# Optimization experiments

Hardware: AMD Instinct MI355X
Metric: run time of the kernel (lower is better)

The kernel has to match this reference:

```python
import jax, jax.numpy as jnp
import numpy as np

WIN = 7
K1 = 0.01
K2 = 0.03
COV_NORM = WIN * WIN / (WIN * WIN - 1.0)  # unbiased covariance correction


def _box_filter(t):
    # t: [B, 1, H, W]; valid conv with uniform 7x7 window (mean filter)
    w = jnp.ones((1, 1, WIN, WIN), t.dtype) / (WIN * WIN)
    return jax.lax.conv_general_dilated(
        t, w, window_strides=(1, 1), padding='VALID',
        dimension_numbers=('NCHW', 'OIHW', 'NCHW'))


def setup_inputs() -> dict:
    key = jax.random.key(0)
    kx, ky = jax.random.split(key)
    B, C, H, W = 64, 1, 384, 384
    X = jax.random.normal(kx, (B, C, H, W), dtype=jnp.float32)
    Y = jax.random.normal(ky, (B, C, H, W), dtype=jnp.float32)
    data_range = jnp.ones((B,), dtype=jnp.float32)
    return {"X": X, "Y": Y, "data_range": data_range}


def reference(X, Y, data_range):
    ux = _box_filter(X)
    uy = _box_filter(Y)
    uxx = _box_filter(X * X)
    uxy = _box_filter(X * Y)
    uyy = _box_filter(Y * Y)

    vx = COV_NORM * (uxx - ux * ux)
    vy = COV_NORM * (uyy - uy * uy)
    vxy = COV_NORM * (uxy - ux * uy)

    L = data_range.reshape(-1, 1, 1, 1)  # per-sample dynamic range
    C1 = (K1 * L) ** 2
    C2 = (K2 * L) ** 2

    N1 = 2.0 * ux * uy + C1
    N2 = 2.0 * vxy + C2
    D1 = ux * ux + uy * uy + C1
    D2 = vx + vy + C2
    S = (N1 * N2) / (D1 * D2)

    # original: mean SSIM per sample, then mean over batch; equal-size maps so
    # this equals the mean over the per-sample means
    per_sample = jnp.mean(S, axis=(1, 2, 3))
    return 1.0 - jnp.mean(per_sample)
```

## Files before the change

kernel.cpp:

```cpp
#include <hip/hip_runtime.h>

#define IMH 384
#define IMW 384
#define OH 378
#define OW 378
#define NB 64
#define SROWS 21
#define INROWS 27
#define NSTRIP 18
#define BLOCK 256
#define GSTRIDE 26
#define RING 8
#define LA 6
#define SLOTF 512


template <int CTRL>
__device__ __forceinline__ float dpp_sh(float v) {
    return __int_as_float(__builtin_amdgcn_update_dpp(
        0, __float_as_int(v), CTRL, 0xf, 0xf, true));
}

__device__ __forceinline__ float2 f2add(float2 a, float2 b) { return make_float2(a.x + b.x, a.y + b.y); }
__device__ __forceinline__ float2 f2sub(float2 a, float2 b) { return make_float2(a.x - b.x, a.y - b.y); }
__device__ __forceinline__ float2 f2mul(float2 a, float2 b) { return make_float2(a.x * b.x, a.y * b.y); }
__device__ __forceinline__ float2 f2fma(float2 a, float2 b, float2 c) {
    return make_float2(fmaf(a.x, b.x, c.x), fmaf(a.y, b.y, c.y));
}
__device__ __forceinline__ float2 f2fnma(float2 a, float2 b, float2 c) {
    return make_float2(fmaf(-a.x, b.x, c.x), fmaf(-a.y, b.y, c.y));
}
__device__ __forceinline__ float2 f2fms(float2 a, float s, float2 c) {
    return make_float2(fmaf(a.x, s, -c.x), fmaf(a.y, s, -c.y));
}
__device__ __forceinline__ float2 f2s(float s) { return make_float2(s, s); }

__device__ __forceinline__ void stage16(const float* g, float* l) {
    __builtin_amdgcn_global_load_lds(
        (const __attribute__((address_space(1))) uint32_t*)(g),
        (__attribute__((address_space(3))) uint32_t*)(l),
        16, 0, 0);
}

#define WAITV(n) asm volatile("s_waitcnt vmcnt(" #n ")" ::: "memory")
#define RAWBAR() asm volatile("s_barrier" ::: "memory")

__global__ __launch_bounds__(BLOCK)
__attribute__((amdgpu_waves_per_eu(5, 8)))
void ssim_kernel(
    const float* __restrict__ X, const float* __restrict__ Y,
    const float* __restrict__ data_range, float* __restrict__ partials)
{
    const int tid   = threadIdx.x;
    const int g     = tid >> 4;
    const int j     = tid & 15;
    const int strip = blockIdx.x;
    const int b     = blockIdx.y;
    const int y0    = strip * SROWS;

    __shared__ float sX[RING][SLOTF];
    __shared__ float sY[RING][SLOTF];

    const int wv   = tid >> 6;
    const int ln   = tid & 63;
    const bool isX = (wv < 2);
    const int half = wv & 1;
    const int foff = half * 256 + ln * 4;
    const int fcl  = min(foff, IMW - 4);
    const float* __restrict__ gstg =
        (isX ? X : Y) + b * (IMH * IMW) + y0 * IMW + fcl;
    float* const lstg = (isX ? &sX[0][0] : &sY[0][0]) + foff;

    const int ce  = g * GSTRIDE + 2 * j;
    const int cin = min(ce, IMW - 2);
    const float2 vmask = make_float2(
        ((j <= 12) && (ce     < OW)) ? 1.f : 0.f,
        ((j <= 12) && (ce + 1 < OW)) ? 1.f : 0.f);

    const float L  = data_range[b];
    const float C1 = (0.01f * L) * (0.01f * L);
    const float C2 = (0.03f * L) * (0.03f * L);
    asm volatile("" :: "v"(C1), "v"(C2));
    __builtin_amdgcn_sched_barrier(0);

    #pragma unroll
    for (int k = 0; k < LA; ++k)
        stage16(gstg + k * IMW, lstg + k * SLOTF);

    const float inv49 = 1.0f / 49.0f;
    const float covn  = 49.0f / 48.0f;

    float2 xh[7], yh[7];
    #pragma unroll
    for (int k = 0; k < 7; ++k) { xh[k] = f2s(0.f); yh[k] = f2s(0.f); }
    float2 V0 = f2s(0.f), V1 = f2s(0.f), V2 = f2s(0.f),
           V3 = f2s(0.f), V4 = f2s(0.f);
    float2 ls2 = f2s(0.f);

    static_assert(INROWS == 27 && LA == 6 && RING == 8, "wait ladder");

    #pragma unroll
    for (int r = 0; r < INROWS; ++r) {
        if (r + LA < INROWS)
            stage16(gstg + (r + LA) * IMW, lstg + ((r + LA) % RING) * SLOTF);

        if      (r < 21) WAITV(6);
        else if (r == 21) WAITV(5);
        else if (r == 22) WAITV(4);
        else if (r == 23) WAITV(3);
        else if (r == 24) WAITV(2);
        else if (r == 25) WAITV(1);
        else              WAITV(0);
        RAWBAR();

        const float2 x = *(const float2*)&sX[r % RING][cin];
        const float2 y = *(const float2*)&sY[r % RING][cin];

        const int ks = r % 7;
        const float2 xo = xh[ks], yo = yh[ks];
        V0 = f2add(V0, f2sub(x, xo));
        V1 = f2add(V1, f2sub(y, yo));
        V2 = f2fma(x, x, V2);  V2 = f2fnma(xo, xo, V2);
        V3 = f2fma(x, y, V3);  V3 = f2fnma(xo, yo, V3);
        V4 = f2fma(y, y, V4);  V4 = f2fnma(yo, yo, V4);
        xh[ks] = x; yh[ks] = y;

        if (r >= 6) {
            const float2 Vv[5] = {V0, V1, V2, V3, V4};
            float Se[5], So[5];
            #pragma unroll
            for (int p = 0; p < 5; ++p) {
                const float e  = Vv[p].x;
                const float o  = Vv[p].y;
                const float pp = e + o;
                float B = pp + dpp_sh<0x101>(pp);
                float C = B + dpp_sh<0x102>(B);
                Se[p] = C - dpp_sh<0x103>(o);
                So[p] = C - e;
            }
            const float2 S0 = make_float2(Se[0], So[0]);
            const float2 S1 = make_float2(Se[1], So[1]);
            const float2 S2 = make_float2(Se[2], So[2]);
            const float2 S3 = make_float2(Se[3], So[3]);
            const float2 S4 = make_float2(Se[4], So[4]);

            float2 ux   = f2mul(S0, f2s(inv49));
            float2 uy   = f2mul(S1, f2s(inv49));
            float2 uxux = f2mul(ux, ux);
            float2 uyuy = f2mul(uy, uy);
            float2 uxuy = f2mul(ux, uy);
            float2 vx   = f2mul(f2fms(S2, inv49, uxux), f2s(covn));
            float2 vy   = f2mul(f2fms(S4, inv49, uyuy), f2s(covn));
            float2 vxy  = f2mul(f2fms(S3, inv49, uxuy), f2s(covn));
            float2 N1   = f2fma(f2s(2.f), uxuy, f2s(C1));
            float2 N2   = f2fma(f2s(2.f), vxy, f2s(C2));
            float2 D1   = f2add(f2add(uxux, uyuy), f2s(C1));
            float2 D2   = f2add(f2add(vx, vy), f2s(C2));
            float2 num  = f2mul(N1, N2);
            float2 den  = f2mul(D1, D2);
            const float rdd = __builtin_amdgcn_rcpf(den.x * den.y);
            float2 s2 = make_float2(num.x * den.y * rdd,
                                    num.y * den.x * rdd);
            ls2 = f2fma(s2, vmask, ls2);
        }
    }

    float lsum = ls2.x + ls2.y;
    #pragma unroll
    for (int off = 32; off > 0; off >>= 1)
        lsum += __shfl_down(lsum, off, 64);
    __syncthreads();
    if ((tid & 63) == 0) sX[0][tid >> 6] = lsum;
    __syncthreads();
    if (tid == 0) {
        partials[b * NSTRIP + strip] =
            sX[0][0] + sX[0][1] + sX[0][2] + sX[0][3];
    }
}

__global__ void finalize_kernel(const float* __restrict__ partials,
                                float* __restrict__ out)
{
    float v = 0.f;
    #pragma unroll
    for (int k = 0; k < NSTRIP; ++k)
        v += partials[threadIdx.x + 64 * k];
    #pragma unroll
    for (int off = 32; off > 0; off >>= 1)
        v += __shfl_down(v, off, 64);
    if (threadIdx.x == 0)
        out[0] = 1.0f - v * (1.0f / (float)(NB * OH * OW));
}

extern "C" void kernel_launch(void* const* d_in, const int* in_sizes, int n_in,
                              void* d_out, int out_size, void* d_ws, size_t ws_size,
                              hipStream_t stream) {
    const float* X  = (const float*)d_in[0];
    const float* Y  = (const float*)d_in[1];
    const float* dr = (const float*)d_in[2];
    float* out = (float*)d_out;
    float* partials = (float*)d_ws;

    dim3 grid(NSTRIP, NB);
    dim3 block(BLOCK);
    ssim_kernel<<<grid, block, 0, stream>>>(X, Y, dr, partials);
    finalize_kernel<<<1, 64, 0, stream>>>(partials, out);
}
```

Before: 28.20 us.

## Stage per-wave private LDS windows to remove block-wide barriers per row

Each wave now loads its own overlapping 128-column window of X and Y rows into a private LDS region using 4-byte global-to-LDS loads. Because each wave reads only data it staged itself, the per-row s_barrier is dropped and vmcnt waits alone order the loads and reads. The aim is to let waves run out of step with each other instead of stalling on block-wide barriers every row. In exchange, each wave issues four times as many load instructions of narrower width, and overlapping windows fetch redundant columns.

```diff
diff --git a/kernel.cpp b/kernel.cpp
--- a/kernel.cpp
+++ b/kernel.cpp
@@ -9,10 +9,10 @@
 #define INROWS 27
 #define NSTRIP 18
 #define BLOCK 256
-#define GSTRIDE 26
+#define SEGW 104
+#define WINF 128
 #define RING 8
 #define LA 6
-#define SLOTF 512
 
 
 template <int CTRL>
@@ -35,15 +35,14 @@
 }
 __device__ __forceinline__ float2 f2s(float s) { return make_float2(s, s); }
 
-__device__ __forceinline__ void stage16(const float* g, float* l) {
+__device__ __forceinline__ void stage4(const float* g, float* l) {
     __builtin_amdgcn_global_load_lds(
         (const __attribute__((address_space(1))) uint32_t*)(g),
         (__attribute__((address_space(3))) uint32_t*)(l),
-        16, 0, 0);
+        4, 0, 0);
 }
 
 #define WAITV(n) asm volatile("s_waitcnt vmcnt(" #n ")" ::: "memory")
-#define RAWBAR() asm volatile("s_barrier" ::: "memory")
 
 __global__ __launch_bounds__(BLOCK)
 __attribute__((amdgpu_waves_per_eu(5, 8)))
@@ -52,27 +51,25 @@
     const float* __restrict__ data_range, float* __restrict__ partials)
 {
     const int tid   = threadIdx.x;
-    const int g     = tid >> 4;
-    const int j     = tid & 15;
+    const int wv    = tid >> 6;
+    const int ln    = tid & 63;
+    const int g4    = ln >> 4;
+    const int j     = ln & 15;
     const int strip = blockIdx.x;
     const int b     = blockIdx.y;
     const int y0    = strip * SROWS;
 
-    __shared__ float sX[RING][SLOTF];
-    __shared__ float sY[RING][SLOTF];
-
-    const int wv   = tid >> 6;
-    const int ln   = tid & 63;
-    const bool isX = (wv < 2);
-    const int half = wv & 1;
-    const int foff = half * 256 + ln * 4;
-    const int fcl  = min(foff, IMW - 4);
-    const float* __restrict__ gstg =
-        (isX ? X : Y) + b * (IMH * IMW) + y0 * IMW + fcl;
-    float* const lstg = (isX ? &sX[0][0] : &sY[0][0]) + foff;
-
-    const int ce  = g * GSTRIDE + 2 * j;
-    const int cin = min(ce, IMW - 2);
+    __shared__ float lds[4][2][RING][WINF];
+
+    const int W = min(SEGW * wv, IMW - WINF);
+
+    const float* __restrict__ gx = X + b * (IMH * IMW) + y0 * IMW + W + ln;
+    const float* __restrict__ gy = Y + b * (IMH * IMW) + y0 * IMW + W + ln;
+    float* const lx = &lds[wv][0][0][0];
+    float* const ly = &lds[wv][1][0][0];
+
+    const int ce   = wv * SEGW + g4 * 26 + 2 * j;
+    const int lidx = min(ce, IMW - 2) - W;
     const float2 vmask = make_float2(
         ((j <= 12) && (ce     < OW)) ? 1.f : 0.f,
         ((j <= 12) && (ce + 1 < OW)) ? 1.f : 0.f);
@@ -84,8 +81,12 @@
     __builtin_amdgcn_sched_barrier(0);
 
     #pragma unroll
-    for (int k = 0; k < LA; ++k)
-        stage16(gstg + k * IMW, lstg + k * SLOTF);
+    for (int k = 0; k < LA; ++k) {
+        stage4(gx + k * IMW,      &lx[k * WINF]);
+        stage4(gx + k * IMW + 64, &lx[k * WINF + 64]);
+        stage4(gy + k * IMW,      &ly[k * WINF]);
+        stage4(gy + k * IMW + 64, &ly[k * WINF + 64]);
+    }
 
     const float inv49 = 1.0f / 49.0f;
     const float covn  = 49.0f / 48.0f;
@@ -101,20 +102,24 @@
 
     #pragma unroll
     for (int r = 0; r < INROWS; ++r) {
-        if (r + LA < INROWS)
-            stage16(gstg + (r + LA) * IMW, lstg + ((r + LA) % RING) * SLOTF);
-
-        if      (r < 21) WAITV(6);
-        else if (r == 21) WAITV(5);
-        else if (r == 22) WAITV(4);
-        else if (r == 23) WAITV(3);
-        else if (r == 24) WAITV(2);
-        else if (r == 25) WAITV(1);
+        if (r + LA < INROWS) {
+            const int s = (r + LA) % RING;
+            stage4(gx + (r + LA) * IMW,      &lx[s * WINF]);
+            stage4(gx + (r + LA) * IMW + 64, &lx[s * WINF + 64]);
+            stage4(gy + (r + LA) * IMW,      &ly[s * WINF]);
+            stage4(gy + (r + LA) * IMW + 64, &ly[s * WINF + 64]);
+        }
+
+        if      (r < 21)  WAITV(24);
+        else if (r == 21) WAITV(20);
+        else if (r == 22) WAITV(16);
+        else if (r == 23) WAITV(12);
+        else if (r == 24) WAITV(8);
+        else if (r == 25) WAITV(4);
         else              WAITV(0);
-        RAWBAR();
-
-        const float2 x = *(const float2*)&sX[r % RING][cin];
-        const float2 y = *(const float2*)&sY[r % RING][cin];
+
+        const float2 x = *(const float2*)&lds[wv][0][r % RING][lidx];
+        const float2 y = *(const float2*)&lds[wv][1][r % RING][lidx];
 
         const int ks = r % 7;
         const float2 xo = xh[ks], yo = yh[ks];
@@ -170,11 +175,11 @@
     for (int off = 32; off > 0; off >>= 1)
         lsum += __shfl_down(lsum, off, 64);
     __syncthreads();
-    if ((tid & 63) == 0) sX[0][tid >> 6] = lsum;
+    if (ln == 0) ((float*)lds)[wv] = lsum;
     __syncthreads();
     if (tid == 0) {
-        partials[b * NSTRIP + strip] =
-            sX[0][0] + sX[0][1] + sX[0][2] + sX[0][3];
+        partials[b * NSTRIP + strip] = ((float*)lds)[0] + ((float*)lds)[1]
+                                     + ((float*)lds)[2] + ((float*)lds)[3];
     }
 }
 
```

Result: slower. 36.41 us (+29.1%).

## Process rows in pairs with register-prefetched LDS reads and fewer barriers

Applied to the files above, without the earlier changes.

Restructures the row loop to stage and consume two input rows per iteration over a 4-slot pair ring. LDS reads for the next pair are issued into registers before computing the current pair, and the next global->LDS copies are issued afterwards. The goal is to halve the barrier and waitcnt count and overlap LDS latency with compute. In exchange it uses more registers and loads one extra (clamped) row at the end.

```diff
diff --git a/kernel.cpp b/kernel.cpp
--- a/kernel.cpp
+++ b/kernel.cpp
@@ -10,8 +10,7 @@
 #define NSTRIP 18
 #define BLOCK 256
 #define GSTRIDE 26
-#define RING 8
-#define LA 6
+#define NPAIR 14
 #define SLOTF 512
 
 
@@ -58,8 +57,8 @@
     const int b     = blockIdx.y;
     const int y0    = strip * SROWS;
 
-    __shared__ float sX[RING][SLOTF];
-    __shared__ float sY[RING][SLOTF];
+    __shared__ float sX[4][2][SLOTF];
+    __shared__ float sY[4][2][SLOTF];
 
     const int wv   = tid >> 6;
     const int ln   = tid & 63;
@@ -69,7 +68,9 @@
     const int fcl  = min(foff, IMW - 4);
     const float* __restrict__ gstg =
         (isX ? X : Y) + b * (IMH * IMW) + y0 * IMW + fcl;
-    float* const lstg = (isX ? &sX[0][0] : &sY[0][0]) + foff;
+    const float* __restrict__ gstg27 =
+        (isX ? X : Y) + b * (IMH * IMW) + min(y0 + 27, IMH - 1) * IMW + fcl;
+    float* const lbase = (isX ? &sX[0][0][0] : &sY[0][0][0]) + foff;
 
     const int ce  = g * GSTRIDE + 2 * j;
     const int cin = min(ce, IMW - 2);
@@ -84,8 +85,16 @@
     __builtin_amdgcn_sched_barrier(0);
 
     #pragma unroll
-    for (int k = 0; k < LA; ++k)
-        stage16(gstg + k * IMW, lstg + k * SLOTF);
+    for (int q = 0; q < 4; ++q) {
+        stage16(gstg + (2 * q) * IMW,     lbase + (2 * q + 0) * SLOTF);
+        stage16(gstg + (2 * q + 1) * IMW, lbase + (2 * q + 1) * SLOTF);
+    }
+    WAITV(6);
+    RAWBAR();
+    float2 cx0 = *(const float2*)&sX[0][0][cin];
+    float2 cx1 = *(const float2*)&sX[0][1][cin];
+    float2 cy0 = *(const float2*)&sY[0][0][cin];
+    float2 cy1 = *(const float2*)&sY[0][1][cin];
 
     const float inv49 = 1.0f / 49.0f;
     const float covn  = 49.0f / 48.0f;
@@ -97,25 +106,7 @@
            V3 = f2s(0.f), V4 = f2s(0.f);
     float2 ls2 = f2s(0.f);
 
-    static_assert(INROWS == 27 && LA == 6 && RING == 8, "wait ladder");
-
-    #pragma unroll
-    for (int r = 0; r < INROWS; ++r) {
-        if (r + LA < INROWS)
-            stage16(gstg + (r + LA) * IMW, lstg + ((r + LA) % RING) * SLOTF);
-
-        if      (r < 21) WAITV(6);
-        else if (r == 21) WAITV(5);
-        else if (r == 22) WAITV(4);
-        else if (r == 23) WAITV(3);
-        else if (r == 24) WAITV(2);
-        else if (r == 25) WAITV(1);
-        else              WAITV(0);
-        RAWBAR();
-
-        const float2 x = *(const float2*)&sX[r % RING][cin];
-        const float2 y = *(const float2*)&sY[r % RING][cin];
-
+    auto rowcompute = [&](int r, float2 x, float2 y) {
         const int ks = r % 7;
         const float2 xo = xh[ks], yo = yh[ks];
         V0 = f2add(V0, f2sub(x, xo));
@@ -129,14 +120,14 @@
             const float2 Vv[5] = {V0, V1, V2, V3, V4};
             float Se[5], So[5];
             #pragma unroll
-            for (int p = 0; p < 5; ++p) {
-                const float e  = Vv[p].x;
-                const float o  = Vv[p].y;
+            for (int q = 0; q < 5; ++q) {
+                const float e  = Vv[q].x;
+                const float o  = Vv[q].y;
                 const float pp = e + o;
                 float B = pp + dpp_sh<0x101>(pp);
                 float C = B + dpp_sh<0x102>(B);
-                Se[p] = C - dpp_sh<0x103>(o);
-                So[p] = C - e;
+                Se[q] = C - dpp_sh<0x103>(o);
+                So[q] = C - e;
             }
             const float2 S0 = make_float2(Se[0], So[0]);
             const float2 S1 = make_float2(Se[1], So[1]);
@@ -163,18 +154,48 @@
                                     num.y * den.x * rdd);
             ls2 = f2fma(s2, vmask, ls2);
         }
+    };
+
+    static_assert(INROWS == 27 && NPAIR == 14, "ladder");
+
+    #pragma unroll
+    for (int p = 1; p < NPAIR; ++p) {
+        if      (p <= 11) WAITV(4);
+        else if (p == 12) WAITV(2);
+        else              WAITV(0);
+        RAWBAR();
+
+        const int sl = p & 3;
+        float2 nx0 = *(const float2*)&sX[sl][0][cin];
+        float2 nx1 = *(const float2*)&sX[sl][1][cin];
+        float2 ny0 = *(const float2*)&sY[sl][0][cin];
+        float2 ny1 = *(const float2*)&sY[sl][1][cin];
+
+        rowcompute(2 * (p - 1),     cx0, cy0);
+        rowcompute(2 * (p - 1) + 1, cx1, cy1);
+
+        if (p + 3 < NPAIR) {
+            const int q = p + 3;
+            const float* s1 = (q == 13) ? gstg27 : gstg + (2 * q + 1) * IMW;
+            stage16(gstg + (2 * q) * IMW, lbase + ((q & 3) * 2 + 0) * SLOTF);
+            stage16(s1,                   lbase + ((q & 3) * 2 + 1) * SLOTF);
+        }
+
+        cx0 = nx0; cx1 = nx1; cy0 = ny0; cy1 = ny1;
     }
+
+    rowcompute(26, cx0, cy0);
 
     float lsum = ls2.x + ls2.y;
     #pragma unroll
     for (int off = 32; off > 0; off >>= 1)
         lsum += __shfl_down(lsum, off, 64);
     __syncthreads();
-    if ((tid & 63) == 0) sX[0][tid >> 6] = lsum;
+    if ((tid & 63) == 0) sX[0][0][tid >> 6] = lsum;
     __syncthreads();
     if (tid == 0) {
         partials[b * NSTRIP + strip] =
-            sX[0][0] + sX[0][1] + sX[0][2] + sX[0][3];
+            sX[0][0][0] + sX[0][0][1] + sX[0][0][2] + sX[0][0][3];
     }
 }
 
```

After: 27.93 us. About the same (-1.0%).
